# Kernel optimization log

Measured on AMD Instinct MI355X. Metric: run time of the kernel, lower is better.

Reference implementation:

```python
import jax, jax.numpy as jnp
import numpy as np

# CogForge GroupedQueryAttention (prefill path): GQA + RoPE + sliding-window+global-token mask
B, T, DM = 2, 2048, 768
H, HKV, DH = 12, 4, 64          # d_head = d_model // n_heads
GROUPS = H // HKV               # kv_groups = 3
WIN, GLB = 512, 64              # window_size, global_tokens
THETA = 10000.0


def _rotate_half(x):
    half = x.shape[-1] // 2
    return jnp.concatenate([-x[..., half:], x[..., :half]], axis=-1)


def _rope_cos_sin(seq_len, dim, dtype):
    inv_freq = 1.0 / (THETA ** (jnp.arange(0, dim, 2, dtype=jnp.float32) / dim))
    t = jnp.arange(seq_len, dtype=jnp.float32)
    freqs = jnp.outer(t, inv_freq)                      # [T, DH/2]
    emb = jnp.concatenate([freqs, freqs], axis=-1)      # [T, DH]
    return jnp.cos(emb).astype(dtype)[None, None], jnp.sin(emb).astype(dtype)[None, None]


def _sparse_mask(seq_len):
    # allowed(i,j) = causal AND (within window OR j is a global token)
    i = jnp.arange(seq_len)[:, None]
    j = jnp.arange(seq_len)[None, :]
    allowed = (j <= i) & (((i - j) < WIN) | (j < GLB))
    return jnp.where(allowed, 0.0, -jnp.inf).astype(jnp.float32)  # [T, T]


def setup_inputs() -> dict:
    key = jax.random.key(0)
    kx, kq, kk, kv, ko = jax.random.split(key, 5)
    x = jax.random.normal(kx, (B, T, DM), jnp.float32)
    wq = jax.random.normal(kq, (DM, H * DH), jnp.float32) * 0.02
    wk = jax.random.normal(kk, (DM, HKV * DH), jnp.float32) * 0.02
    wv = jax.random.normal(kv, (DM, HKV * DH), jnp.float32) * 0.02
    wo = jax.random.normal(ko, (H * DH, DM), jnp.float32) * 0.02
    return {"x": x, "wq": wq, "wk": wk, "wv": wv, "wo": wo}


def reference(x, wq, wk, wv, wo):
    # projections -> [B, heads, T, DH]
    q = (x @ wq).reshape(B, T, H, DH).transpose(0, 2, 1, 3)
    k = (x @ wk).reshape(B, T, HKV, DH).transpose(0, 2, 1, 3)
    v = (x @ wv).reshape(B, T, HKV, DH).transpose(0, 2, 1, 3)

    cos, sin = _rope_cos_sin(T, DH, x.dtype)            # [1,1,T,DH]
    q = q * cos + _rotate_half(q) * sin
    k = k * cos + _rotate_half(k) * sin

    # expand kv heads to match query heads (GQA)
    k = jnp.repeat(k, GROUPS, axis=1)                   # [B,H,T,DH]
    v = jnp.repeat(v, GROUPS, axis=1)

    scale = 1.0 / jnp.sqrt(jnp.asarray(DH, x.dtype))
    scores = jnp.einsum('bhtd,bhsd->bhts', q, k) * scale
    scores = scores + _sparse_mask(T)[None, None]
    weights = jax.nn.softmax(scores, axis=-1)           # attn_dropout = 0.0

    out = jnp.einsum('bhts,bhsd->bhtd', weights, v)
    out = out.transpose(0, 2, 1, 3).reshape(B, T, H * DH)
    return out @ wo
```

## Files before the change

kernel.cpp:

```cpp
#include <hip/hip_runtime.h>
#include <hip/hip_bf16.h>


typedef __attribute__((ext_vector_type(8))) short bf16x8;
typedef __attribute__((ext_vector_type(4))) short bf16x4;
typedef __attribute__((ext_vector_type(4))) float f32x4;
typedef __attribute__((ext_vector_type(4))) unsigned short u16x4;

#define MFMA   __builtin_amdgcn_mfma_f32_16x16x32_bf16
#define MFMA16 __builtin_amdgcn_mfma_f32_16x16x16bf16_1k

constexpr int BB = 2, TT = 2048, DM = 768, HH = 12, HKV = 4, DH = 64;
constexpr int WIN = 512, GLB = 64;
constexpr float SC2 = 0.18033688011112042f;

__device__ __forceinline__ unsigned short f2b(float f) {
    union { float f; unsigned int u; } v; v.f = f;
    unsigned int r = v.u + 0x7fffu + ((v.u >> 16) & 1u);
    return (unsigned short)(r >> 16);
}

#define GLOAD_LDS(gp, lp)                                                      \
    __builtin_amdgcn_global_load_lds(                                          \
        (const __attribute__((address_space(1))) void*)(gp),                   \
        (__attribute__((address_space(3))) void*)(lp), 16, 0, 0)

__global__ __launch_bounds__(256) void k_pre(const float* __restrict__ x,
                                             unsigned short* __restrict__ xb,
                                             float2* __restrict__ rope,
                                             const float* __restrict__ wq,
                                             const float* __restrict__ wk,
                                             const float* __restrict__ wv,
                                             const float* __restrict__ wo,
                                             unsigned short* __restrict__ wqT,
                                             unsigned short* __restrict__ wkT,
                                             unsigned short* __restrict__ wvT,
                                             unsigned short* __restrict__ woT) {
    __shared__ float t[32][33];
    int bid = blockIdx.x, tid = threadIdx.x;
    if (bid < 3072) {
        int i = bid * 256 + tid;
        float4 v = ((const float4*)x)[i];
        u16x4 o; o.x = f2b(v.x); o.y = f2b(v.y); o.z = f2b(v.z); o.w = f2b(v.w);
        ((u16x4*)xb)[i] = o;
        return;
    }
    if (bid < 3328) {
        int i = (bid - 3072) * 256 + tid;
        int tt = i >> 5, p = i & 31;
        float inv = exp2f(-(float)p * (13.287712379549449f / 32.0f));
        float ang = (float)tt * inv;
        rope[i] = make_float2(cosf(ang), sinf(ang));
        return;
    }
    int wb = bid - 3328;
    const float* src; unsigned short* dst; int N, tile;
    if (wb < 576)      { src = wq; dst = wqT; N = 768; tile = wb; }
    else if (wb < 768) { src = wk; dst = wkT; N = 256; tile = wb - 576; }
    else if (wb < 960) { src = wv; dst = wvT; N = 256; tile = wb - 768; }
    else               { src = wo; dst = woT; N = 768; tile = wb - 960; }
    int ntiles = N / 32;
    int k0 = (tile / ntiles) * 32, n0 = (tile % ntiles) * 32;
    int tx = tid & 31, ty = tid >> 5;
    #pragma unroll
    for (int e = 0; e < 4; ++e) {
        int r = ty + e * 8;
        t[r][tx] = src[(size_t)(k0 + r) * N + n0 + tx];
    }
    __syncthreads();
    #pragma unroll
    for (int e = 0; e < 4; ++e) {
        int r = ty + e * 8;
        dst[(size_t)(n0 + r) * DM + k0 + tx] = f2b(t[tx][r]);
    }
}

__global__ __launch_bounds__(256) void k_qkv(const unsigned short* __restrict__ xb,
                                             const unsigned short* __restrict__ wqT,
                                             const unsigned short* __restrict__ wkT,
                                             const unsigned short* __restrict__ wvT,
                                             unsigned short* __restrict__ qb,
                                             unsigned short* __restrict__ kb,
                                             unsigned short* __restrict__ vtb,
                                             const float2* __restrict__ rope) {
    __shared__ __align__(16) unsigned short Ab[2][128 * 64];
    __shared__ __align__(16) unsigned short Bb[2][64 * 64];
    const int tid = threadIdx.x;
    const int wave = tid >> 6, lane = tid & 63;
    const int quad = lane >> 4, col = lane & 15;
    const int y = blockIdx.y;
    int mode, hl;
    const unsigned short* Bt;
    if (y < 12)      { mode = 0; hl = y;      Bt = wqT + (size_t)hl * 64 * DM; }
    else if (y < 16) { mode = 1; hl = y - 12; Bt = wkT + (size_t)hl * 64 * DM; }
    else             { mode = 2; hl = y - 16; Bt = wvT + (size_t)hl * 64 * DM; }
    const int m0b = blockIdx.x * 128;

    const int rg = lane >> 3;
    const int cg = (lane & 7) ^ rg;
    const int ck = col & 7;

    f32x4 acc[2][4];
    #pragma unroll
    for (int rt = 0; rt < 2; ++rt)
        #pragma unroll
        for (int j = 0; j < 4; ++j) acc[rt][j] = f32x4{0.f, 0.f, 0.f, 0.f};

    auto stage = [&](int buf, int k) {
        #pragma unroll
        for (int m = 0; m < 4; ++m) {
            int g = wave * 4 + m;
            GLOAD_LDS(xb + (size_t)(m0b + g * 8 + rg) * DM + k + cg * 8,
                      &Ab[buf][g * 512]);
        }
        #pragma unroll
        for (int m = 0; m < 2; ++m) {
            int g = wave * 2 + m;
            GLOAD_LDS(Bt + (size_t)(g * 8 + rg) * DM + k + cg * 8,
                      &Bb[buf][g * 512]);
        }
    };

    stage(0, 0);
    __syncthreads();

    const int arow0 = (wave * 32 + col) * 64;
    const int arow1 = (wave * 32 + 16 + col) * 64;

    for (int t = 0; t < 12; ++t) {
        const int buf = t & 1;
        if (t < 11) stage(buf ^ 1, (t + 1) * 64);
        __builtin_amdgcn_s_setprio(1);
        #pragma unroll
        for (int ks = 0; ks < 2; ++ks) {
            const int p = ((ks * 4 + quad) ^ ck) * 8;
            bf16x8 a0 = *(const bf16x8*)&Ab[buf][arow0 + p];
            bf16x8 a1 = *(const bf16x8*)&Ab[buf][arow1 + p];
            #pragma unroll
            for (int j = 0; j < 4; ++j) {
                bf16x8 b = *(const bf16x8*)&Bb[buf][(j * 16 + col) * 64 + p];
                acc[0][j] = MFMA(a0, b, acc[0][j], 0, 0, 0);
                acc[1][j] = MFMA(a1, b, acc[1][j], 0, 0, 0);
            }
        }
        __builtin_amdgcn_s_setprio(0);
        __syncthreads();
    }

    if (mode == 2) {
        int b = m0b >> 11;
        #pragma unroll
        for (int j = 0; j < 4; ++j)
            #pragma unroll
            for (int rt = 0; rt < 2; ++rt)
                #pragma unroll
                for (int r = 0; r < 4; ++r) {
                    int m = m0b + wave * 32 + rt * 16 + quad * 4 + r;
                    int t = m & (TT - 1);
                    int d = j * 16 + col;
                    vtb[((size_t)(b * HKV + hl) * DH + d) * TT + t] = f2b(acc[rt][j][r]);
                }
        return;
    }
    int nheads = (mode == 0) ? HH : HKV;
    unsigned short* ob = (mode == 0) ? qb : kb;
    #pragma unroll
    for (int rt = 0; rt < 2; ++rt)
        #pragma unroll
        for (int r = 0; r < 4; ++r) {
            int m = m0b + wave * 32 + rt * 16 + quad * 4 + r;
            int t = m & (TT - 1);
            int b = m >> 11;
            float2 cs0 = rope[t * 32 + col];
            float2 cs1 = rope[t * 32 + 16 + col];
            float v0 = acc[rt][0][r], v1 = acc[rt][1][r], v2 = acc[rt][2][r], v3 = acc[rt][3][r];
            unsigned short* dst = ob + ((size_t)(b * nheads + hl) * TT + t) * DH + col;
            dst[0]  = f2b(v0 * cs0.x - v2 * cs0.y);
            dst[16] = f2b(v1 * cs1.x - v3 * cs1.y);
            dst[32] = f2b(v2 * cs0.x + v0 * cs0.y);
            dst[48] = f2b(v3 * cs1.x + v1 * cs1.y);
        }
}

__global__ __launch_bounds__(256) void k_out(const unsigned short* __restrict__ ao,
                                             const unsigned short* __restrict__ woT,
                                             float* __restrict__ out) {
    __shared__ __align__(16) unsigned short Ab[2][128 * 64];
    __shared__ __align__(16) unsigned short Bb[2][64 * 64];
    const int tid = threadIdx.x;
    const int wave = tid >> 6, lane = tid & 63;
    const int quad = lane >> 4, col = lane & 15;
    const int m0b = blockIdx.x * 128;
    const int n0 = blockIdx.y * 64;

    const int rg = lane >> 3;
    const int cg = (lane & 7) ^ rg;
    const int ck = col & 7;

    f32x4 acc[2][4];
    #pragma unroll
    for (int rt = 0; rt < 2; ++rt)
        #pragma unroll
        for (int j = 0; j < 4; ++j) acc[rt][j] = f32x4{0.f, 0.f, 0.f, 0.f};

    auto stage = [&](int buf, int k) {
        #pragma unroll
        for (int m = 0; m < 4; ++m) {
            int g = wave * 4 + m;
            GLOAD_LDS(ao + (size_t)(m0b + g * 8 + rg) * DM + k + cg * 8,
                      &Ab[buf][g * 512]);
        }
        #pragma unroll
        for (int m = 0; m < 2; ++m) {
            int g = wave * 2 + m;
            GLOAD_LDS(woT + (size_t)(n0 + g * 8 + rg) * DM + k + cg * 8,
                      &Bb[buf][g * 512]);
        }
    };

    stage(0, 0);
    __syncthreads();

    const int arow0 = (wave * 32 + col) * 64;
    const int arow1 = (wave * 32 + 16 + col) * 64;

    for (int t = 0; t < 12; ++t) {
        const int buf = t & 1;
        if (t < 11) stage(buf ^ 1, (t + 1) * 64);
        __builtin_amdgcn_s_setprio(1);
        #pragma unroll
        for (int ks = 0; ks < 2; ++ks) {
            const int p = ((ks * 4 + quad) ^ ck) * 8;
            bf16x8 a0 = *(const bf16x8*)&Ab[buf][arow0 + p];
            bf16x8 a1 = *(const bf16x8*)&Ab[buf][arow1 + p];
            #pragma unroll
            for (int j = 0; j < 4; ++j) {
                bf16x8 b = *(const bf16x8*)&Bb[buf][(j * 16 + col) * 64 + p];
                acc[0][j] = MFMA(a0, b, acc[0][j], 0, 0, 0);
                acc[1][j] = MFMA(a1, b, acc[1][j], 0, 0, 0);
            }
        }
        __builtin_amdgcn_s_setprio(0);
        __syncthreads();
    }

    #pragma unroll
    for (int rt = 0; rt < 2; ++rt)
        #pragma unroll
        for (int j = 0; j < 4; ++j)
            #pragma unroll
            for (int r = 0; r < 4; ++r) {
                int m = m0b + wave * 32 + rt * 16 + quad * 4 + r;
                out[(size_t)m * DM + n0 + j * 16 + col] = acc[rt][j][r];
            }
}

__global__ __launch_bounds__(256) void k_attn(const unsigned short* __restrict__ Q,
                                              const unsigned short* __restrict__ K,
                                              const unsigned short* __restrict__ Vt,
                                              unsigned short* __restrict__ AO) {
    __shared__ __align__(16) unsigned short kbuf[2][64 * 64];
    __shared__ __align__(16) unsigned short vbuf[2][64 * 64];
    const int lane = threadIdx.x & 63;
    const int wave = threadIdx.x >> 6;
    const int quad = lane >> 4, col = lane & 15;
    const int lbid = (blockIdx.x & 7) * 96 + (blockIdx.x >> 3);
    const int qb = lbid & 31, bh = lbid >> 5;
    const int h = bh % HH, b = bh / HH;
    const int hkv = h / 3;
    const int i0 = qb * 64 + wave * 16;
    const int irow = i0 + col;

    const unsigned short* qbase = Q + ((size_t)(b * HH + h) * TT + irow) * DH + quad * 8;
    const bf16x8 qf0 = *(const bf16x8*)qbase;
    const bf16x8 qf1 = *(const bf16x8*)(qbase + 32);
    const unsigned short* kbase = K + (size_t)(b * HKV + hkv) * TT * DH;
    const unsigned short* vbase = Vt + (size_t)(b * HKV + hkv) * DH * TT;

    float m_run = -1e30f, l_lane = 0.f;
    f32x4 accO[4];
    #pragma unroll
    for (int dt = 0; dt < 4; ++dt) accO[dt] = f32x4{0.f, 0.f, 0.f, 0.f};

    int jw0 = (qb * 64 - WIN + 1) & ~63; if (jw0 < 64) jw0 = 64;
    const int jlast = qb * 64;
    const int nt = 1 + ((jlast >= 64) ? (((jlast - jw0) >> 6) + 1) : 0);
    auto j0_of = [&](int t) { return (t == 0) ? 0 : (jw0 + ((t - 1) << 6)); };

    const int sr = lane >> 3;
    const int soff = ((lane & 7) ^ sr) * 8;
    const int ck = col & 7;

    auto stage = [&](int bb, int j0) {
        GLOAD_LDS(kbase + (size_t)(j0 + wave * 16 + sr) * DH + soff,
                  &kbuf[bb][(wave * 16) * 64]);
        GLOAD_LDS(kbase + (size_t)(j0 + wave * 16 + 8 + sr) * DH + soff,
                  &kbuf[bb][(wave * 16 + 8) * 64]);
        GLOAD_LDS(vbase + (size_t)(wave * 16 + sr) * TT + j0 + soff,
                  &vbuf[bb][(wave * 16) * 64]);
        GLOAD_LDS(vbase + (size_t)(wave * 16 + 8 + sr) * TT + j0 + soff,
                  &vbuf[bb][(wave * 16 + 8) * 64]);
    };

    stage(0, 0);
    __syncthreads();

    for (int t = 0; t < nt; ++t) {
        const int bb = t & 1;
        if (t + 1 < nt) stage(bb ^ 1, j0_of(t + 1));

        const int j0 = j0_of(t);
        const int mode = (t == 0) ? ((i0 < 64) ? 1 : 0)
                       : (((j0 + 63 > i0) || (j0 <= i0 + 15 - WIN)) ? 2 : 0);

        f32x4 sT[4];
        #pragma unroll
        for (int f = 0; f < 4; ++f) sT[f] = f32x4{0.f, 0.f, 0.f, 0.f};
        __builtin_amdgcn_s_setprio(1);
        #pragma unroll
        for (int f = 0; f < 4; ++f) {
            bf16x8 k0 = *(const bf16x8*)&kbuf[bb][(f * 16 + col) * 64 + (quad ^ ck) * 8];
            bf16x8 k1 = *(const bf16x8*)&kbuf[bb][(f * 16 + col) * 64 + ((4 + quad) ^ ck) * 8];
            sT[f] = MFMA(k0, qf0, sT[f], 0, 0, 0);
            sT[f] = MFMA(k1, qf1, sT[f], 0, 0, 0);
        }
        __builtin_amdgcn_s_setprio(0);

        const int dq = irow - j0 - quad * 4;
        if (mode == 1) {
            #pragma unroll
            for (int f = 0; f < 4; ++f)
                #pragma unroll
                for (int r = 0; r < 4; ++r)
                    if (dq - f * 16 - r < 0) sT[f][r] = -3e30f;
        } else if (mode == 2) {
            #pragma unroll
            for (int f = 0; f < 4; ++f)
                #pragma unroll
                for (int r = 0; r < 4; ++r)
                    if ((unsigned)(dq - f * 16 - r) >= (unsigned)WIN) sT[f][r] = -3e30f;
        }

        float mx = -3e30f;
        #pragma unroll
        for (int f = 0; f < 4; ++f)
            #pragma unroll
            for (int r = 0; r < 4; ++r) mx = fmaxf(mx, sT[f][r]);

        if (!__all(mx <= m_run + 44.f)) {
            float rm = fmaxf(mx, __shfl_xor(mx, 16));
            rm = fmaxf(rm, __shfl_xor(rm, 32));
            float mn = fmaxf(m_run, rm);
            float corr = exp2f((m_run - mn) * SC2);
            m_run = mn;
            l_lane *= corr;
            #pragma unroll
            for (int dt = 0; dt < 4; ++dt)
                #pragma unroll
                for (int r = 0; r < 4; ++r) accO[dt][r] *= corr;
        }

        const float mbase = m_run * SC2;
        unsigned int pk[4][2];
        float ps = 0.f;
        #pragma unroll
        for (int f = 0; f < 4; ++f) {
            float p0 = exp2f(__builtin_fmaf(sT[f][0], SC2, -mbase));
            float p1 = exp2f(__builtin_fmaf(sT[f][1], SC2, -mbase));
            float p2 = exp2f(__builtin_fmaf(sT[f][2], SC2, -mbase));
            float p3 = exp2f(__builtin_fmaf(sT[f][3], SC2, -mbase));
            ps += (p0 + p1) + (p2 + p3);
            asm("v_cvt_pk_bf16_f32 %0, %1, %2" : "=v"(pk[f][0]) : "v"(p0), "v"(p1));
            asm("v_cvt_pk_bf16_f32 %0, %1, %2" : "=v"(pk[f][1]) : "v"(p2), "v"(p3));
        }
        l_lane += ps;

        __builtin_amdgcn_s_setprio(1);
        #pragma unroll
        for (int f = 0; f < 4; ++f) {
            union { bf16x4 v; unsigned int u[2]; } pb;
            pb.u[0] = pk[f][0];
            pb.u[1] = pk[f][1];
            const int voff = (((2 * f + (quad >> 1)) ^ ck) << 3) + ((quad & 1) << 2);
            #pragma unroll
            for (int dt = 0; dt < 4; ++dt) {
                bf16x4 va = *(const bf16x4*)&vbuf[bb][(dt * 16 + col) * 64 + voff];
                accO[dt] = MFMA16(va, pb.v, accO[dt], 0, 0, 0);
            }
        }
        __builtin_amdgcn_s_setprio(0);

        __syncthreads();
    }

    float lr = l_lane;
    lr += __shfl_xor(lr, 16);
    lr += __shfl_xor(lr, 32);
    const float inv = 1.0f / lr;

    unsigned short* dst = AO + ((size_t)b * TT + irow) * DM + h * DH + quad * 4;
    #pragma unroll
    for (int dt = 0; dt < 4; ++dt) {
        u16x4 o;
        o.x = f2b(accO[dt][0] * inv);
        o.y = f2b(accO[dt][1] * inv);
        o.z = f2b(accO[dt][2] * inv);
        o.w = f2b(accO[dt][3] * inv);
        *(u16x4*)(dst + dt * 16) = o;
    }
}

extern "C" void kernel_launch(void* const* d_in, const int* in_sizes, int n_in,
                              void* d_out, int out_size, void* d_ws, size_t ws_size,
                              hipStream_t stream) {
    const float* x  = (const float*)d_in[0];
    const float* wq = (const float*)d_in[1];
    const float* wk = (const float*)d_in[2];
    const float* wv = (const float*)d_in[3];
    const float* wo = (const float*)d_in[4];
    float* out = (float*)d_out;

    char* ws = (char*)d_ws;
    size_t off = 0;
    auto alloc = [&](size_t bytes) -> void* {
        void* p = ws + off;
        off += (bytes + 255) & ~(size_t)255;
        return p;
    };
    const int M = BB * TT;
    unsigned short* xb  = (unsigned short*)alloc((size_t)M * DM * 2);
    unsigned short* wqT = (unsigned short*)alloc((size_t)DM * DM * 2);
    unsigned short* wkT = (unsigned short*)alloc((size_t)(HKV * DH) * DM * 2);
    unsigned short* wvT = (unsigned short*)alloc((size_t)(HKV * DH) * DM * 2);
    unsigned short* woT = (unsigned short*)alloc((size_t)DM * DM * 2);
    unsigned short* qb  = (unsigned short*)alloc((size_t)BB * HH * TT * DH * 2);
    unsigned short* kb  = (unsigned short*)alloc((size_t)BB * HKV * TT * DH * 2);
    unsigned short* vtb = (unsigned short*)alloc((size_t)BB * HKV * DH * TT * 2);
    unsigned short* ao  = (unsigned short*)alloc((size_t)M * DM * 2);
    float2* rope        = (float2*)alloc((size_t)TT * 32 * sizeof(float2));

    k_pre<<<4864, 256, 0, stream>>>(x, xb, rope, wq, wk, wv, wo, wqT, wkT, wvT, woT);
    k_qkv<<<dim3(M / 128, 20), 256, 0, stream>>>(xb, wqT, wkT, wvT, qb, kb, vtb, rope);
    k_attn<<<768, 256, 0, stream>>>(qb, kb, vtb, ao);
    k_out<<<dim3(M / 128, 12), 256, 0, stream>>>(ao, woT, out);
}
```

Measured before the change: 61.66 us.

## Triple-buffer LDS staging with explicit vmcnt waits in GEMM and attention kernels

Switches the QKV GEMM, output GEMM and attention kernels from double to triple buffering of LDS tiles. Each iteration prefetches two tiles ahead and waits with an explicit s_waitcnt vmcnt on only the older loads, followed by a single barrier, in place of the previous full __syncthreads at the end of each iteration. The goal is to hide global-to-LDS latency and cut one barrier per iteration. It costs more LDS per block, which may lower occupancy, and depends on the vmcnt counts matching the number of loads issued per stage.

```diff
diff --git a/kernel.cpp b/kernel.cpp
--- a/kernel.cpp
+++ b/kernel.cpp
@@ -24,6 +24,9 @@
     __builtin_amdgcn_global_load_lds(                                          \
         (const __attribute__((address_space(1))) void*)(gp),                   \
         (__attribute__((address_space(3))) void*)(lp), 16, 0, 0)
+
+#define WAIT_VM(N)                                                             \
+    asm volatile("s_waitcnt vmcnt(" #N ")" ::: "memory")
 
 __global__ __launch_bounds__(256) void k_pre(const float* __restrict__ x,
                                              unsigned short* __restrict__ xb,
@@ -83,8 +86,8 @@
                                              unsigned short* __restrict__ kb,
                                              unsigned short* __restrict__ vtb,
                                              const float2* __restrict__ rope) {
-    __shared__ __align__(16) unsigned short Ab[2][128 * 64];
-    __shared__ __align__(16) unsigned short Bb[2][64 * 64];
+    __shared__ __align__(16) unsigned short Ab[3][128 * 64];
+    __shared__ __align__(16) unsigned short Bb[3][64 * 64];
     const int tid = threadIdx.x;
     const int wave = tid >> 6, lane = tid & 63;
     const int quad = lane >> 4, col = lane & 15;
@@ -122,14 +125,17 @@
     };
 
     stage(0, 0);
-    __syncthreads();
+    stage(1, 64);
 
     const int arow0 = (wave * 32 + col) * 64;
     const int arow1 = (wave * 32 + 16 + col) * 64;
 
     for (int t = 0; t < 12; ++t) {
-        const int buf = t & 1;
-        if (t < 11) stage(buf ^ 1, (t + 1) * 64);
+        const int buf = t % 3;
+        if (t < 11) WAIT_VM(6); else WAIT_VM(0);
+        __builtin_amdgcn_s_barrier();
+        __builtin_amdgcn_sched_barrier(0);
+        if (t + 2 < 12) stage((t + 2) % 3, (t + 2) * 64);
         __builtin_amdgcn_s_setprio(1);
         #pragma unroll
         for (int ks = 0; ks < 2; ++ks) {
@@ -144,7 +150,6 @@
             }
         }
         __builtin_amdgcn_s_setprio(0);
-        __syncthreads();
     }
 
     if (mode == 2) {
@@ -185,8 +190,8 @@
 __global__ __launch_bounds__(256) void k_out(const unsigned short* __restrict__ ao,
                                              const unsigned short* __restrict__ woT,
                                              float* __restrict__ out) {
-    __shared__ __align__(16) unsigned short Ab[2][128 * 64];
-    __shared__ __align__(16) unsigned short Bb[2][64 * 64];
+    __shared__ __align__(16) unsigned short Ab[3][128 * 64];
+    __shared__ __align__(16) unsigned short Bb[3][64 * 64];
     const int tid = threadIdx.x;
     const int wave = tid >> 6, lane = tid & 63;
     const int quad = lane >> 4, col = lane & 15;
@@ -219,14 +224,17 @@
     };
 
     stage(0, 0);
-    __syncthreads();
+    stage(1, 64);
 
     const int arow0 = (wave * 32 + col) * 64;
     const int arow1 = (wave * 32 + 16 + col) * 64;
 
     for (int t = 0; t < 12; ++t) {
-        const int buf = t & 1;
-        if (t < 11) stage(buf ^ 1, (t + 1) * 64);
+        const int buf = t % 3;
+        if (t < 11) WAIT_VM(6); else WAIT_VM(0);
+        __builtin_amdgcn_s_barrier();
+        __builtin_amdgcn_sched_barrier(0);
+        if (t + 2 < 12) stage((t + 2) % 3, (t + 2) * 64);
         __builtin_amdgcn_s_setprio(1);
         #pragma unroll
         for (int ks = 0; ks < 2; ++ks) {
@@ -241,7 +249,6 @@
             }
         }
         __builtin_amdgcn_s_setprio(0);
-        __syncthreads();
     }
 
     #pragma unroll
@@ -259,8 +266,8 @@
                                               const unsigned short* __restrict__ K,
                                               const unsigned short* __restrict__ Vt,
                                               unsigned short* __restrict__ AO) {
-    __shared__ __align__(16) unsigned short kbuf[2][64 * 64];
-    __shared__ __align__(16) unsigned short vbuf[2][64 * 64];
+    __shared__ __align__(16) unsigned short kbuf[3][64 * 64];
+    __shared__ __align__(16) unsigned short vbuf[3][64 * 64];
     const int lane = threadIdx.x & 63;
     const int wave = threadIdx.x >> 6;
     const int quad = lane >> 4, col = lane & 15;
@@ -303,11 +310,14 @@
     };
 
     stage(0, 0);
-    __syncthreads();
+    if (nt > 1) stage(1, j0_of(1));
 
     for (int t = 0; t < nt; ++t) {
-        const int bb = t & 1;
-        if (t + 1 < nt) stage(bb ^ 1, j0_of(t + 1));
+        const int bb = t % 3;
+        if (t + 1 < nt) WAIT_VM(4); else WAIT_VM(0);
+        __builtin_amdgcn_s_barrier();
+        __builtin_amdgcn_sched_barrier(0);
+        if (t + 2 < nt) stage((t + 2) % 3, j0_of(t + 2));
 
         const int j0 = j0_of(t);
         const int mode = (t == 0) ? ((i0 < 64) ? 1 : 0)
@@ -389,8 +399,6 @@
             }
         }
         __builtin_amdgcn_s_setprio(0);
-
-        __syncthreads();
     }
 
     float lr = l_lane;
```

Result: slower. 68.38 us (+10.9%).
